# Optimization experiments

Measured on AMD Instinct MI355X. Metric: run time of the kernel, lower is better.

## Reference

```python
import jax, jax.numpy as jnp
import numpy as np

B, S, D, H, DH = 4, 2048, 1024, 16, 64
INIT_STD = 0.02
IGNORE = -100000.0


def setup_inputs() -> dict:
    key = jax.random.key(0)
    ks = jax.random.split(key, 5)
    x = jax.random.normal(ks[0], (B, S, D), dtype=jnp.float32)
    W_Q = INIT_STD * jax.random.normal(ks[1], (H, D, DH), dtype=jnp.float32)
    W_K = INIT_STD * jax.random.normal(ks[2], (H, D, DH), dtype=jnp.float32)
    W_V = INIT_STD * jax.random.normal(ks[3], (H, D, DH), dtype=jnp.float32)
    W_O = INIT_STD * jax.random.normal(ks[4], (H, DH, D), dtype=jnp.float32)
    b_Q = jnp.zeros((H, DH), dtype=jnp.float32)
    b_K = jnp.zeros((H, DH), dtype=jnp.float32)
    b_V = jnp.zeros((H, DH), dtype=jnp.float32)
    b_O = jnp.zeros((D,), dtype=jnp.float32)
    return {"x": x, "W_Q": W_Q, "b_Q": b_Q, "W_K": W_K, "b_K": b_K,
            "W_V": W_V, "b_V": b_V, "W_O": W_O, "b_O": b_O}


def reference(x, W_Q, b_Q, W_K, b_K, W_V, b_V, W_O, b_O):
    # x: (B, S, D); projections -> (B, S, H, DH)
    Q = jnp.einsum('bqd,hde->bqhe', x, W_Q) + b_Q
    K = jnp.einsum('bkd,hde->bkhe', x, W_K) + b_K
    V = jnp.einsum('bkd,hde->bkhe', x, W_V) + b_V
    d_head = Q.shape[-1]
    # scores: (B, H, Sq, Sk)
    scores = jnp.einsum('bqhe,bkhe->bhqk', Q, K) / np.sqrt(d_head).astype(np.float32)
    s = scores.shape[-1]
    causal = jnp.triu(jnp.ones((s, s), dtype=bool), k=1)
    scores = jnp.where(causal, jnp.float32(IGNORE), scores)
    A = jax.nn.softmax(scores, axis=-1)
    z = jnp.einsum('bhqk,bkhe->bqhe', A, V)
    # output projection: sum over heads + bias
    attn_out = jnp.einsum('bqhe,hed->bqd', z, W_O) + b_O
    return attn_out
```

## Files before the change

### kernel.cpp

```cpp
#include <hip/hip_runtime.h>


#define B_ 4
#define S_ 2048
#define D_ 1024
#define H_ 16
#define DH_ 64

typedef unsigned short ushort_t;
typedef __attribute__((ext_vector_type(4))) short short4v;
typedef __attribute__((ext_vector_type(8))) short short8v;
typedef __attribute__((ext_vector_type(4))) float floatx4;
typedef __attribute__((ext_vector_type(4))) unsigned short ushort4v;

static __device__ __forceinline__ ushort_t f2bf(float f) {
    union { float f; unsigned u; } v; v.f = f;
    unsigned r = v.u + 0x7fffu + ((v.u >> 16) & 1u);
    return (ushort_t)(r >> 16);
}

static __device__ __forceinline__ float fast_exp2(float x) {
#if __has_builtin(__builtin_amdgcn_exp2f)
    return __builtin_amdgcn_exp2f(x);
#else
    return exp2f(x);
#endif
}

static __device__ __forceinline__ unsigned pack_bf16_tr(float lo, float hi) {
    union { float f; unsigned u; } a, b;
    a.f = lo; b.f = hi;
    return __builtin_amdgcn_perm(b.u, a.u, 0x07060302u);
}

static __device__ __forceinline__ void g2lds16(const void* g, void* l) {
    __builtin_amdgcn_global_load_lds(
        (__attribute__((address_space(1))) void*)(unsigned long long)(size_t)g,
        (__attribute__((address_space(3))) void*)(unsigned int)(size_t)l,
        16, 0, 0);
}

__global__ void prep_kernel(const float* __restrict__ x,
                            const float* __restrict__ wq, const float* __restrict__ wk,
                            const float* __restrict__ wv, const float* __restrict__ wo,
                            ushort_t* __restrict__ xb, ushort_t* __restrict__ wt,
                            ushort_t* __restrict__ wot) {
    __shared__ float tile[32][33];
    int bid = blockIdx.x;
    int tid = threadIdx.x;
    if (bid < 8192) {
        int i = (bid * 256 + tid) * 4;
        float4 v = *(const float4*)&x[i];
        ushort4v o;
        o[0] = f2bf(v.x); o[1] = f2bf(v.y); o[2] = f2bf(v.z); o[3] = f2bf(v.w);
        *(ushort4v*)&xb[i] = o;
        return;
    }
    const float* src;
    ushort_t* d;
    int C, r0, c0;
    if (bid < 11264) {
        int t = bid - 8192;
        int z = t / 64, r = t % 64;
        src = (z < 16 ? wq : (z < 32 ? wk : wv)) + (size_t)(z & 15) * 65536;
        d = wt + (size_t)z * 65536;
        C = 64; r0 = (r >> 1) * 32; c0 = (r & 1) * 32;
    } else {
        int t = bid - 11264;
        int z = t / 64, r = t % 64;
        src = wo + (size_t)z * 65536;
        d = wot + (size_t)z * 64;
        C = 1024; r0 = (r & 1) * 32; c0 = (r >> 1) * 32;
    }
    int tx = tid & 31, ty = tid >> 5;
#pragma unroll
    for (int i = 0; i < 4; ++i)
        tile[ty + i * 8][tx] = src[(size_t)(r0 + ty + i * 8) * C + c0 + tx];
    __syncthreads();
#pragma unroll
    for (int i = 0; i < 4; ++i)
        d[(size_t)(c0 + ty + i * 8) * 1024 + r0 + tx] = f2bf(tile[tx][ty + i * 8]);
}


#define GQ_BAR() __builtin_amdgcn_s_barrier()
#define GQ_VM4 do { asm volatile("s_waitcnt vmcnt(4)"); __builtin_amdgcn_sched_barrier(0); } while (0)
#define GQ_VM2 do { asm volatile("s_waitcnt vmcnt(2)"); __builtin_amdgcn_sched_barrier(0); } while (0)
#define GQ_VM0 do { asm volatile("s_waitcnt vmcnt(0)"); __builtin_amdgcn_sched_barrier(0); } while (0)
#define GQ_WAITLG do { asm volatile("s_waitcnt lgkmcnt(0)"); __builtin_amdgcn_sched_barrier(0); } while (0)

#define GQ_READS_B(KB)                                                          \
    _Pragma("unroll") for (int nt = 0; nt < 4; ++nt)                            \
        bfr[KB][nt] = *(const short8v*)&cB[(wn * 64 + nt * 16) * 64 + ((KB) ? kb1 : kb0)];

#define GQ_READS_A(MH, KB)                                                      \
    _Pragma("unroll") for (int i = 0; i < 2; ++i)                               \
        af[i] = *(const short8v*)&cA[(wm * 64 + ((MH) * 2 + i) * 16) * 64 + ((KB) ? kb1 : kb0)];

#define GQ_MFMA(MH, KB)                                                         \
    GQ_WAITLG;                                                                  \
    __builtin_amdgcn_s_setprio(1);                                              \
    _Pragma("unroll") for (int i = 0; i < 2; ++i)                               \
        _Pragma("unroll") for (int nt = 0; nt < 4; ++nt)                        \
            acc[(MH) * 2 + i][nt] = __builtin_amdgcn_mfma_f32_16x16x32_bf16(    \
                af[i], bfr[KB][nt], acc[(MH) * 2 + i][nt], 0, 0, 0);            \
    __builtin_amdgcn_s_setprio(0);                                              \
    __builtin_amdgcn_sched_barrier(0);

#define GQ_KSTEP(CA, CB, S1, S2, S3, S4, WMID, WEND) do {                       \
    const ushort_t* cA = (CA); const ushort_t* cB = (CB);                       \
    short8v af[2]; short8v bfr[2][4];                                           \
    GQ_READS_B(0) GQ_READS_A(0, 0) S1; GQ_BAR();                                \
    GQ_MFMA(0, 0) GQ_BAR();                                                     \
    GQ_READS_B(1) GQ_READS_A(0, 1) S2; GQ_BAR();                                \
    GQ_MFMA(0, 1) WMID; GQ_BAR();                                               \
    GQ_READS_A(1, 0) S3; GQ_BAR();                                              \
    GQ_MFMA(1, 0) GQ_BAR();                                                     \
    GQ_READS_A(1, 1) S4; GQ_BAR();                                              \
    GQ_MFMA(1, 1) WEND; GQ_BAR();                                               \
} while (0)

#define GQ_RUN()                                                                \
    stA(sA[0], 0, uA); stA(sA[0], 0, uA + 8);                                   \
    stB(sB[0], 0, bR); stB(sB[0], 0, bR + 8);                                   \
    stB(sB[0], 0, bR + 16); stB(sB[0], 0, bR + 24);                             \
    stA(sA[0], 0, uA + 32); stA(sA[0], 0, uA + 40);                             \
    GQ_VM2;                                                                     \
    GQ_BAR();                                                                   \
    int p = 0;                                                                  \
    for (int t = 0; t < 15; ++t) {                                              \
        const int kk = (t + 1) * 64;                                            \
        ushort_t* nA = sA[p ^ 1];                                               \
        ushort_t* nB = sB[p ^ 1];                                               \
        GQ_KSTEP(sA[p], sB[p],                                                  \
                 { stA(nA, kk, uA); stA(nA, kk, uA + 8); },                     \
                 { stB(nB, kk, bR); stB(nB, kk, bR + 8); },                     \
                 { stB(nB, kk, bR + 16); stB(nB, kk, bR + 24); },               \
                 { stA(nA, kk, uA + 32); stA(nA, kk, uA + 40); },               \
                 GQ_VM4, GQ_VM2);                                               \
        p ^= 1;                                                                 \
    }                                                                           \
    GQ_KSTEP(sA[1], sB[1], (void)0, (void)0, (void)0, (void)0, GQ_VM0, (void)0);

__global__ __launch_bounds__(256, 2) void gemm_qkv(const ushort_t* __restrict__ A,
                                                   const ushort_t* __restrict__ Wt,
                                                   const float* __restrict__ bq,
                                                   const float* __restrict__ bk,
                                                   const float* __restrict__ bv,
                                                   ushort_t* __restrict__ Qw,
                                                   ushort_t* __restrict__ Kw,
                                                   ushort_t* __restrict__ Vw) {
    __shared__ ushort_t sA[2][128 * 64];
    __shared__ ushort_t sB[2][128 * 64];
    const int tid = threadIdx.x;
    const int lane = tid & 63, w = tid >> 6;
    const int lq = lane & 15, quad = lane >> 4;
    const int wm = w >> 1, wn = w & 1;
    const int m0 = blockIdx.x * 128, n0 = blockIdx.y * 128;

    const int kb0 = lq * 64 + ((quad ^ (lq & 7)) << 3);
    const int kb1 = lq * 64 + (((4 | quad) ^ (lq & 7)) << 3);

    const int uA = ((w >> 1) << 6) + ((w & 1) << 4);
    const int bR = w * 32;

    auto stA = [&](ushort_t* dst, int kk, int R0) __attribute__((always_inline)) {
        int rr = R0 + (lane >> 3);
        int cc = (lane & 7) ^ (rr & 7);
        g2lds16(&A[(size_t)(m0 + rr) * 1024 + kk + cc * 8], &dst[R0 * 64]);
    };
    auto stB = [&](ushort_t* dst, int kk, int R0) __attribute__((always_inline)) {
        int rr = R0 + (lane >> 3);
        int cc = (lane & 7) ^ (rr & 7);
        g2lds16(&Wt[(size_t)(n0 + rr) * 1024 + kk + cc * 8], &dst[R0 * 64]);
    };

    floatx4 acc[4][4] = {};

    GQ_RUN()

    const int mat = blockIdx.y >> 3;
    const float* bias = mat == 0 ? bq : (mat == 1 ? bk : bv);
    const int colbase = (blockIdx.y & 7) * 128 + wn * 64;
    float bias_v[4];
#pragma unroll
    for (int nt = 0; nt < 4; ++nt) bias_v[nt] = bias[colbase + nt * 16 + lq];

#pragma unroll
    for (int mt = 0; mt < 4; ++mt) {
#pragma unroll
        for (int nt = 0; nt < 4; ++nt) {
            int row0 = m0 + wm * 64 + mt * 16 + quad * 4;
            int col = colbase + nt * 16 + lq;
            int h = col >> 6, e = col & 63;
            if (mat == 2) {
                int b = row0 >> 11, s = row0 & 2047;
                ushort4v pk;
#pragma unroll
                for (int rg = 0; rg < 4; ++rg) pk[rg] = f2bf(acc[mt][nt][rg] + bias_v[nt]);
                *(ushort4v*)&Vw[((size_t)((b << 4) | h) * 64 + e) * 2048 + s] = pk;
            } else {
                ushort_t* Du = mat == 0 ? Qw : Kw;
#pragma unroll
                for (int rg = 0; rg < 4; ++rg) {
                    int row = row0 + rg;
                    int b = row >> 11, s = row & 2047;
                    float v = acc[mt][nt][rg] + bias_v[nt];
                    if (mat == 0) v *= 0.18033688011112042f;
                    Du[((size_t)((b << 4) | h) * 2048 + s) * 64 + e] = f2bf(v);
                }
            }
        }
    }
}

__global__ __launch_bounds__(256) void attn_kernel(const ushort_t* __restrict__ Q,
                                                   const ushort_t* __restrict__ Kg,
                                                   const ushort_t* __restrict__ Vt,
                                                   ushort_t* __restrict__ Z) {
    __shared__ ushort_t sK[2][128 * 64];
    __shared__ ushort_t sV[2][64 * 128];
    const int tid = threadIdx.x;
    const int lane = tid & 63, w = tid >> 6;
    const int lq = lane & 15, quad = lane >> 4;
    const int bh = blockIdx.x;
    const int b = bh >> 4, h = bh & 15;
    const ushort_t* Qp = Q + (size_t)bh * S_ * DH_;
    const ushort_t* Kp = Kg + (size_t)bh * S_ * DH_;
    const ushort_t* Vp = Vt + (size_t)bh * DH_ * S_;

    const int kbase0 = lq * 64 + ((quad ^ (lq & 7)) << 3);
    const int kbase1 = lq * 64 + (((4 | quad) ^ (lq & 7)) << 3);
    const int vbase2 = lq * 128 + quad * 4;
    const int vko = (lq & 7) << 4;

    const floatx4 fzero = {0.f, 0.f, 0.f, 0.f};

    auto stageK = [&](int kt, int bs) __attribute__((always_inline)) {
        ushort_t* dK = sK[bs];
#pragma unroll
        for (int p = 0; p < 4; ++p) {
            int rrk = w * 32 + p * 8 + (lane >> 3);
            int ck = (lane & 7) ^ (rrk & 7);
            g2lds16(&Kp[(size_t)(kt * 128 + rrk) * 64 + ck * 8], &dK[(w * 32 + p * 8) * 64]);
        }
    };
    auto stageV = [&](int kt, int bs) __attribute__((always_inline)) {
        ushort_t* dV = sV[bs];
#pragma unroll
        for (int p = 0; p < 4; ++p) {
            int R0 = w * 16 + p * 4;
            int e = R0 + (lane >> 4);
            int u = lane & 15;
            int usw = ((((u >> 1) ^ (e & 7)) << 1) | (u & 1));
            g2lds16(&Vp[(size_t)e * 2048 + kt * 128 + usw * 8], &dV[R0 * 128]);
        }
    };

    for (int pass = 0; pass < 2; ++pass) {
        const int qt = pass == 0 ? (int)blockIdx.y : 15 - (int)blockIdx.y;
        const int q0 = qt * 128;

        short8v qf[2][2];
#pragma unroll
        for (int qi = 0; qi < 2; ++qi)
#pragma unroll
            for (int ks = 0; ks < 2; ++ks)
                qf[qi][ks] = *(const short8v*)&Qp[(size_t)(q0 + w * 32 + qi * 16 + lq) * DH_ + ks * 32 + quad * 8];

        float l_i[2] = {0.f, 0.f};
        floatx4 o[2][4] = {};

        __syncthreads();
        stageK(0, 0);
        stageV(0, 0);

        for (int kt = 0; kt <= qt; ++kt) {
            const bool diag = (kt == qt);
            const ushort_t* cK = sK[kt & 1];
            const ushort_t* cV = sV[kt & 1];

            __syncthreads();
            if (kt < qt) {
                stageK(kt + 1, (kt + 1) & 1);
                stageV(kt + 1, (kt + 1) & 1);
            }

            floatx4 st[8][2];
#pragma unroll
            for (int si = 0; si < 8; ++si) {
                short8v a0 = *(const short8v*)&cK[kbase0 + si * 1024];
                short8v a1 = *(const short8v*)&cK[kbase1 + si * 1024];
#pragma unroll
                for (int qi = 0; qi < 2; ++qi) {
                    st[si][qi] = __builtin_amdgcn_mfma_f32_16x16x32_bf16(a0, qf[qi][0], fzero, 0, 0, 0);
                    st[si][qi] = __builtin_amdgcn_mfma_f32_16x16x32_bf16(a1, qf[qi][1], st[si][qi], 0, 0, 0);
                }
            }

            short4v pf[8][2];
#pragma unroll
            for (int qi = 0; qi < 2; ++qi) {
                const int qg = q0 + w * 32 + qi * 16 + lq;
                float lsum = 0.f;
#pragma unroll
                for (int si = 0; si < 8; ++si) {
                    float p[4];
#pragma unroll
                    for (int rg = 0; rg < 4; ++rg) {
                        float v = st[si][qi][rg];
                        if (diag) {
                            int sg = kt * 128 + si * 16 + quad * 4 + rg;
                            if (sg > qg) v = -1e30f;
                        }
                        p[rg] = fast_exp2(v);
                        lsum += p[rg];
                    }
                    union { unsigned u[2]; short4v v4; } pk;
                    pk.u[0] = pack_bf16_tr(p[0], p[1]);
                    pk.u[1] = pack_bf16_tr(p[2], p[3]);
                    pf[si][qi] = pk.v4;
                }
                l_i[qi] += lsum;
            }

#pragma unroll
            for (int ksp = 0; ksp < 8; ++ksp) {
                const ushort_t* pV = &cV[vbase2 + ((ksp << 4) ^ vko)];
#pragma unroll
                for (int et = 0; et < 4; ++et) {
                    short4v vf = *(const short4v*)&pV[et * 2048];
#pragma unroll
                    for (int qi = 0; qi < 2; ++qi)
                        o[qi][et] = __builtin_amdgcn_mfma_f32_16x16x16bf16_1k(pf[ksp][qi], vf, o[qi][et], 0, 0, 0);
                }
            }
        }

#pragma unroll
        for (int qi = 0; qi < 2; ++qi) {
            float lf = l_i[qi];
            lf += __shfl_xor(lf, 16);
            lf += __shfl_xor(lf, 32);
            float linv[4];
#pragma unroll
            for (int rg = 0; rg < 4; ++rg) linv[rg] = 1.0f / __shfl(lf, quad * 4 + rg);
#pragma unroll
            for (int et = 0; et < 4; ++et) {
#pragma unroll
                for (int rg = 0; rg < 4; ++rg) {
                    int qg = q0 + w * 32 + qi * 16 + quad * 4 + rg;
                    int e = et * 16 + lq;
                    Z[((size_t)(b * S_ + qg) * H_ + h) * DH_ + e] = f2bf(o[qi][et][rg] * linv[rg]);
                }
            }
        }
    }
}

__global__ __launch_bounds__(256, 2) void gemm_o(const ushort_t* __restrict__ A,
                                                 const ushort_t* __restrict__ Bt,
                                                 const float* __restrict__ bias,
                                                 float* __restrict__ Dst) {
    __shared__ ushort_t sA[2][128 * 64];
    __shared__ ushort_t sB[2][128 * 64];
    const int tid = threadIdx.x;
    const int lane = tid & 63, w = tid >> 6;
    const int lq = lane & 15, quad = lane >> 4;
    const int wm = w >> 1, wn = w & 1;
    const int m0 = blockIdx.x * 128, n0 = blockIdx.y * 128;

    const int kb0 = lq * 64 + ((quad ^ (lq & 7)) << 3);
    const int kb1 = lq * 64 + (((4 | quad) ^ (lq & 7)) << 3);
    const int uA = ((w >> 1) << 6) + ((w & 1) << 4);
    const int bR = w * 32;

    auto stA = [&](ushort_t* dst, int kk, int R0) __attribute__((always_inline)) {
        int rr = R0 + (lane >> 3);
        int cc = (lane & 7) ^ (rr & 7);
        g2lds16(&A[(size_t)(m0 + rr) * 1024 + kk + cc * 8], &dst[R0 * 64]);
    };
    auto stB = [&](ushort_t* dst, int kk, int R0) __attribute__((always_inline)) {
        int rr = R0 + (lane >> 3);
        int cc = (lane & 7) ^ (rr & 7);
        g2lds16(&Bt[(size_t)(n0 + rr) * 1024 + kk + cc * 8], &dst[R0 * 64]);
    };

    floatx4 acc[4][4] = {};

    GQ_RUN()

    const int colbase = n0 + wn * 64;
    float bias_v[4];
#pragma unroll
    for (int nt = 0; nt < 4; ++nt) bias_v[nt] = bias[colbase + nt * 16 + lq];

#pragma unroll
    for (int mt = 0; mt < 4; ++mt) {
#pragma unroll
        for (int nt = 0; nt < 4; ++nt) {
            int row0 = m0 + wm * 64 + mt * 16 + quad * 4;
            int col = colbase + nt * 16 + lq;
#pragma unroll
            for (int rg = 0; rg < 4; ++rg)
                Dst[(size_t)(row0 + rg) * 1024 + col] = acc[mt][nt][rg] + bias_v[nt];
        }
    }
}

extern "C" void kernel_launch(void* const* d_in, const int* in_sizes, int n_in,
                              void* d_out, int out_size, void* d_ws, size_t ws_size,
                              hipStream_t stream) {
    const float* x  = (const float*)d_in[0];
    const float* wq = (const float*)d_in[1];
    const float* bq = (const float*)d_in[2];
    const float* wk = (const float*)d_in[3];
    const float* bk = (const float*)d_in[4];
    const float* wv = (const float*)d_in[5];
    const float* bv = (const float*)d_in[6];
    const float* wo = (const float*)d_in[7];
    const float* bo = (const float*)d_in[8];

    char* ws = (char*)d_ws;
    size_t off = 0;
    ushort_t* xb  = (ushort_t*)(ws + off); off += (size_t)8192 * 1024 * 2;
    ushort_t* wt  = (ushort_t*)(ws + off); off += (size_t)3 * 1024 * 1024 * 2;
    ushort_t* wot = (ushort_t*)(ws + off); off += (size_t)1024 * 1024 * 2;
    ushort_t* Qw  = (ushort_t*)(ws + off); off += (size_t)8192 * 1024 * 2;
    ushort_t* Kw  = (ushort_t*)(ws + off); off += (size_t)8192 * 1024 * 2;
    ushort_t* Vw  = (ushort_t*)(ws + off); off += (size_t)8192 * 1024 * 2;
    ushort_t* Zw  = (ushort_t*)(ws + off); off += (size_t)8192 * 1024 * 2;

    prep_kernel<<<12288, 256, 0, stream>>>(x, wq, wk, wv, wo, xb, wt, wot);
    gemm_qkv<<<dim3(64, 24), 256, 0, stream>>>(xb, wt, bq, bk, bv, Qw, Kw, Vw);
    attn_kernel<<<dim3(64, 8), 256, 0, stream>>>(Qw, Kw, Vw, Zw);
    gemm_o<<<dim3(64, 8), 256, 0, stream>>>(Zw, wot, bo, (float*)d_out);
}
```

Baseline: 246.7 us.

## Fuse fp32-to-bf16 conversion of x into QKV GEMM A-tile loading

Removes the separate conversion pass over x in the prep kernel and its bf16 workspace buffer; the QKV GEMM now loads fp32 x through registers, converts to bf16 and writes swizzled LDS tiles. This eliminates a full read/write pass of the activations. In exchange each GEMM block reads twice as many bytes for A, repeated across all column blocks, and loses the direct global-to-LDS path for A, raising register use and changing the pipeline's wait structure.

```diff
diff --git a/kernel.cpp b/kernel.cpp
--- a/kernel.cpp
+++ b/kernel.cpp
@@ -1,4 +1,8 @@
 #include <hip/hip_runtime.h>
+#if __has_include(<hip/hip_bf16.h>)
+#include <hip/hip_bf16.h>
+#define HAVE_HIP_BF16 1
+#endif
 
 
 #define B_ 4
@@ -17,6 +21,22 @@
     union { float f; unsigned u; } v; v.f = f;
     unsigned r = v.u + 0x7fffu + ((v.u >> 16) & 1u);
     return (ushort_t)(r >> 16);
+}
+
+static __device__ __forceinline__ short8v cvt8(float4 a, float4 b) {
+#ifdef HAVE_HIP_BF16
+    union { short8v v; __hip_bfloat162 h[4]; } r;
+    r.h[0] = __float22bfloat162_rn(make_float2(a.x, a.y));
+    r.h[1] = __float22bfloat162_rn(make_float2(a.z, a.w));
+    r.h[2] = __float22bfloat162_rn(make_float2(b.x, b.y));
+    r.h[3] = __float22bfloat162_rn(make_float2(b.z, b.w));
+    return r.v;
+#else
+    union { short8v v; ushort_t s[8]; } r;
+    r.s[0] = f2bf(a.x); r.s[1] = f2bf(a.y); r.s[2] = f2bf(a.z); r.s[3] = f2bf(a.w);
+    r.s[4] = f2bf(b.x); r.s[5] = f2bf(b.y); r.s[6] = f2bf(b.z); r.s[7] = f2bf(b.w);
+    return r.v;
+#endif
 }
 
 static __device__ __forceinline__ float fast_exp2(float x) {
@@ -40,33 +60,22 @@
         16, 0, 0);
 }
 
-__global__ void prep_kernel(const float* __restrict__ x,
-                            const float* __restrict__ wq, const float* __restrict__ wk,
+__global__ void prep_kernel(const float* __restrict__ wq, const float* __restrict__ wk,
                             const float* __restrict__ wv, const float* __restrict__ wo,
-                            ushort_t* __restrict__ xb, ushort_t* __restrict__ wt,
-                            ushort_t* __restrict__ wot) {
+                            ushort_t* __restrict__ wt, ushort_t* __restrict__ wot) {
     __shared__ float tile[32][33];
     int bid = blockIdx.x;
     int tid = threadIdx.x;
-    if (bid < 8192) {
-        int i = (bid * 256 + tid) * 4;
-        float4 v = *(const float4*)&x[i];
-        ushort4v o;
-        o[0] = f2bf(v.x); o[1] = f2bf(v.y); o[2] = f2bf(v.z); o[3] = f2bf(v.w);
-        *(ushort4v*)&xb[i] = o;
-        return;
-    }
     const float* src;
     ushort_t* d;
     int C, r0, c0;
-    if (bid < 11264) {
-        int t = bid - 8192;
-        int z = t / 64, r = t % 64;
+    if (bid < 3072) {
+        int z = bid / 64, r = bid % 64;
         src = (z < 16 ? wq : (z < 32 ? wk : wv)) + (size_t)(z & 15) * 65536;
         d = wt + (size_t)z * 65536;
         C = 64; r0 = (r >> 1) * 32; c0 = (r & 1) * 32;
     } else {
-        int t = bid - 11264;
+        int t = bid - 3072;
         int z = t / 64, r = t % 64;
         src = wo + (size_t)z * 65536;
         d = wot + (size_t)z * 64;
@@ -142,7 +151,7 @@
     }                                                                           \
     GQ_KSTEP(sA[1], sB[1], (void)0, (void)0, (void)0, (void)0, GQ_VM0, (void)0);
 
-__global__ __launch_bounds__(256, 2) void gemm_qkv(const ushort_t* __restrict__ A,
+__global__ __launch_bounds__(256, 2) void gemm_qkv(const float* __restrict__ X,
                                                    const ushort_t* __restrict__ Wt,
                                                    const float* __restrict__ bq,
                                                    const float* __restrict__ bk,
@@ -164,10 +173,29 @@
     const int uA = ((w >> 1) << 6) + ((w & 1) << 4);
     const int bR = w * 32;
 
-    auto stA = [&](ushort_t* dst, int kk, int R0) __attribute__((always_inline)) {
-        int rr = R0 + (lane >> 3);
-        int cc = (lane & 7) ^ (rr & 7);
-        g2lds16(&A[(size_t)(m0 + rr) * 1024 + kk + cc * 8], &dst[R0 * 64]);
+    const int arow = uA + (lane & 15);
+    const int ac8 = (lane >> 4) * 2;
+    const int asw0 = ((ac8 ^ (arow & 7)) << 3);
+    const int asw1 = (((ac8 + 1) ^ (arow & 7)) << 3);
+
+    float4 ald[8];
+    auto issueA = [&](int kk) __attribute__((always_inline)) {
+        const float* base = &X[(size_t)(m0 + arow) * 1024 + kk + ac8 * 8];
+        ald[0] = *(const float4*)base;
+        ald[1] = *(const float4*)(base + 4);
+        ald[2] = *(const float4*)(base + 8);
+        ald[3] = *(const float4*)(base + 12);
+        const float* lbase = base + 32 * 1024;
+        ald[4] = *(const float4*)lbase;
+        ald[5] = *(const float4*)(lbase + 4);
+        ald[6] = *(const float4*)(lbase + 8);
+        ald[7] = *(const float4*)(lbase + 12);
+    };
+    auto writeA = [&](ushort_t* dst) __attribute__((always_inline)) {
+        *(short8v*)&dst[arow * 64 + asw0] = cvt8(ald[0], ald[1]);
+        *(short8v*)&dst[arow * 64 + asw1] = cvt8(ald[2], ald[3]);
+        *(short8v*)&dst[(arow + 32) * 64 + asw0] = cvt8(ald[4], ald[5]);
+        *(short8v*)&dst[(arow + 32) * 64 + asw1] = cvt8(ald[6], ald[7]);
     };
     auto stB = [&](ushort_t* dst, int kk, int R0) __attribute__((always_inline)) {
         int rr = R0 + (lane >> 3);
@@ -177,7 +205,29 @@
 
     floatx4 acc[4][4] = {};
 
-    GQ_RUN()
+    issueA(0);
+    stB(sB[0], 0, bR); stB(sB[0], 0, bR + 8);
+    stB(sB[0], 0, bR + 16); stB(sB[0], 0, bR + 24);
+    GQ_VM4;
+    writeA(sA[0]);
+    GQ_WAITLG;
+    GQ_VM0;
+    GQ_BAR();
+
+    int p = 0;
+    for (int t = 0; t < 15; ++t) {
+        const int kk = (t + 1) * 64;
+        ushort_t* nA = sA[p ^ 1];
+        ushort_t* nB = sB[p ^ 1];
+        GQ_KSTEP(sA[p], sB[p],
+                 { issueA(kk); },
+                 { stB(nB, kk, bR); stB(nB, kk, bR + 8); },
+                 { stB(nB, kk, bR + 16); stB(nB, kk, bR + 24); GQ_VM4; writeA(nA); },
+                 { },
+                 (void)0, GQ_VM0);
+        p ^= 1;
+    }
+    GQ_KSTEP(sA[1], sB[1], (void)0, (void)0, (void)0, (void)0, (void)0, (void)0);
 
     const int mat = blockIdx.y >> 3;
     const float* bias = mat == 0 ? bq : (mat == 1 ? bk : bv);
@@ -423,7 +473,6 @@
 
     char* ws = (char*)d_ws;
     size_t off = 0;
-    ushort_t* xb  = (ushort_t*)(ws + off); off += (size_t)8192 * 1024 * 2;
     ushort_t* wt  = (ushort_t*)(ws + off); off += (size_t)3 * 1024 * 1024 * 2;
     ushort_t* wot = (ushort_t*)(ws + off); off += (size_t)1024 * 1024 * 2;
     ushort_t* Qw  = (ushort_t*)(ws + off); off += (size_t)8192 * 1024 * 2;
@@ -431,8 +480,8 @@
     ushort_t* Vw  = (ushort_t*)(ws + off); off += (size_t)8192 * 1024 * 2;
     ushort_t* Zw  = (ushort_t*)(ws + off); off += (size_t)8192 * 1024 * 2;
 
-    prep_kernel<<<12288, 256, 0, stream>>>(x, wq, wk, wv, wo, xb, wt, wot);
-    gemm_qkv<<<dim3(64, 24), 256, 0, stream>>>(xb, wt, bq, bk, bv, Qw, Kw, Vw);
+    prep_kernel<<<4096, 256, 0, stream>>>(wq, wk, wv, wo, wt, wot);
+    gemm_qkv<<<dim3(64, 24), 256, 0, stream>>>(x, wt, bq, bk, bv, Qw, Kw, Vw);
     attn_kernel<<<dim3(64, 8), 256, 0, stream>>>(Qw, Kw, Vw, Zw);
     gemm_o<<<dim3(64, 8), 256, 0, stream>>>(Zw, wot, bo, (float*)d_out);
 }
```

After: 301.8 us. 1.22x slower.

## Use eight waves per block in QKV GEMM with smaller per-wave tiles

Applied to the files above, without the earlier changes.

The QKV projection GEMM goes from 256 to 512 threads per block, splitting the 128x128 tile over a 2x4 wave grid so each wave computes 64x32 instead of 64x64. The global-to-LDS loads are redistributed so each wave issues fewer copies per k-step, with waitcnt thresholds adjusted to match. This aims to raise the number of resident waves and hide latency better, at the cost of fewer MFMAs per LDS read and more barrier traffic per wave.

```diff
diff --git a/kernel.cpp b/kernel.cpp
--- a/kernel.cpp
+++ b/kernel.cpp
@@ -85,7 +85,9 @@
 
 #define GQ_BAR() __builtin_amdgcn_s_barrier()
 #define GQ_VM4 do { asm volatile("s_waitcnt vmcnt(4)"); __builtin_amdgcn_sched_barrier(0); } while (0)
+#define GQ_VM3 do { asm volatile("s_waitcnt vmcnt(3)"); __builtin_amdgcn_sched_barrier(0); } while (0)
 #define GQ_VM2 do { asm volatile("s_waitcnt vmcnt(2)"); __builtin_amdgcn_sched_barrier(0); } while (0)
+#define GQ_VM1 do { asm volatile("s_waitcnt vmcnt(1)"); __builtin_amdgcn_sched_barrier(0); } while (0)
 #define GQ_VM0 do { asm volatile("s_waitcnt vmcnt(0)"); __builtin_amdgcn_sched_barrier(0); } while (0)
 #define GQ_WAITLG do { asm volatile("s_waitcnt lgkmcnt(0)"); __builtin_amdgcn_sched_barrier(0); } while (0)
 
@@ -142,7 +144,38 @@
     }                                                                           \
     GQ_KSTEP(sA[1], sB[1], (void)0, (void)0, (void)0, (void)0, GQ_VM0, (void)0);
 
-__global__ __launch_bounds__(256, 2) void gemm_qkv(const ushort_t* __restrict__ A,
+#define GQ8_READS_B(KB)                                                         \
+    _Pragma("unroll") for (int nt = 0; nt < 2; ++nt)                            \
+        bfr[KB][nt] = *(const short8v*)&cB[(wn * 32 + nt * 16) * 64 + ((KB) ? kb1 : kb0)];
+
+#define GQ8_READS_A(MH, KB)                                                     \
+    _Pragma("unroll") for (int i = 0; i < 2; ++i)                               \
+        af[i] = *(const short8v*)&cA[(wm * 64 + ((MH) * 2 + i) * 16) * 64 + ((KB) ? kb1 : kb0)];
+
+#define GQ8_MFMA(MH, KB)                                                        \
+    GQ_WAITLG;                                                                  \
+    __builtin_amdgcn_s_setprio(1);                                              \
+    _Pragma("unroll") for (int i = 0; i < 2; ++i)                               \
+        _Pragma("unroll") for (int nt = 0; nt < 2; ++nt)                        \
+            acc[(MH) * 2 + i][nt] = __builtin_amdgcn_mfma_f32_16x16x32_bf16(    \
+                af[i], bfr[KB][nt], acc[(MH) * 2 + i][nt], 0, 0, 0);            \
+    __builtin_amdgcn_s_setprio(0);                                              \
+    __builtin_amdgcn_sched_barrier(0);
+
+#define GQ8_KSTEP(CA, CB, S1, S2, S3, WMID, WEND) do {                          \
+    const ushort_t* cA = (CA); const ushort_t* cB = (CB);                       \
+    short8v af[2]; short8v bfr[2][2];                                           \
+    GQ8_READS_B(0) GQ8_READS_A(0, 0) S1; GQ_BAR();                              \
+    GQ8_MFMA(0, 0) GQ_BAR();                                                    \
+    GQ8_READS_B(1) GQ8_READS_A(0, 1) S2; GQ_BAR();                              \
+    GQ8_MFMA(0, 1) WMID; GQ_BAR();                                              \
+    GQ8_READS_A(1, 0) S3; GQ_BAR();                                             \
+    GQ8_MFMA(1, 0) GQ_BAR();                                                    \
+    GQ8_READS_A(1, 1) GQ_BAR();                                                 \
+    GQ8_MFMA(1, 1) WEND; GQ_BAR();                                              \
+} while (0)
+
+__global__ __launch_bounds__(512, 2) void gemm_qkv(const ushort_t* __restrict__ A,
                                                    const ushort_t* __restrict__ Wt,
                                                    const float* __restrict__ bq,
                                                    const float* __restrict__ bk,
@@ -155,14 +188,14 @@
     const int tid = threadIdx.x;
     const int lane = tid & 63, w = tid >> 6;
     const int lq = lane & 15, quad = lane >> 4;
-    const int wm = w >> 1, wn = w & 1;
+    const int wm = w >> 2, wn = w & 3;
     const int m0 = blockIdx.x * 128, n0 = blockIdx.y * 128;
 
     const int kb0 = lq * 64 + ((quad ^ (lq & 7)) << 3);
     const int kb1 = lq * 64 + (((4 | quad) ^ (lq & 7)) << 3);
 
-    const int uA = ((w >> 1) << 6) + ((w & 1) << 4);
-    const int bR = w * 32;
+    const int uA = ((w >> 2) << 6) + ((w & 3) << 3);
+    const int bR = w * 16;
 
     auto stA = [&](ushort_t* dst, int kk, int R0) __attribute__((always_inline)) {
         int rr = R0 + (lane >> 3);
@@ -175,21 +208,39 @@
         g2lds16(&Wt[(size_t)(n0 + rr) * 1024 + kk + cc * 8], &dst[R0 * 64]);
     };
 
-    floatx4 acc[4][4] = {};
-
-    GQ_RUN()
+    floatx4 acc[4][2] = {};
+
+    stA(sA[0], 0, uA);
+    stB(sB[0], 0, bR); stB(sB[0], 0, bR + 8);
+    stA(sA[0], 0, uA + 32);
+    GQ_VM1;
+    GQ_BAR();
+
+    int p = 0;
+    for (int t = 0; t < 15; ++t) {
+        const int kk = (t + 1) * 64;
+        ushort_t* nA = sA[p ^ 1];
+        ushort_t* nB = sB[p ^ 1];
+        GQ8_KSTEP(sA[p], sB[p],
+                  { stA(nA, kk, uA); },
+                  { stB(nB, kk, bR); stB(nB, kk, bR + 8); },
+                  { stA(nA, kk, uA + 32); },
+                  GQ_VM3, GQ_VM1);
+        p ^= 1;
+    }
+    GQ8_KSTEP(sA[1], sB[1], (void)0, (void)0, (void)0, GQ_VM0, (void)0);
 
     const int mat = blockIdx.y >> 3;
     const float* bias = mat == 0 ? bq : (mat == 1 ? bk : bv);
-    const int colbase = (blockIdx.y & 7) * 128 + wn * 64;
-    float bias_v[4];
-#pragma unroll
-    for (int nt = 0; nt < 4; ++nt) bias_v[nt] = bias[colbase + nt * 16 + lq];
+    const int colbase = (blockIdx.y & 7) * 128 + wn * 32;
+    float bias_v[2];
+#pragma unroll
+    for (int nt = 0; nt < 2; ++nt) bias_v[nt] = bias[colbase + nt * 16 + lq];
 
 #pragma unroll
     for (int mt = 0; mt < 4; ++mt) {
 #pragma unroll
-        for (int nt = 0; nt < 4; ++nt) {
+        for (int nt = 0; nt < 2; ++nt) {
             int row0 = m0 + wm * 64 + mt * 16 + quad * 4;
             int col = colbase + nt * 16 + lq;
             int h = col >> 6, e = col & 63;
@@ -432,7 +483,7 @@
     ushort_t* Zw  = (ushort_t*)(ws + off); off += (size_t)8192 * 1024 * 2;
 
     prep_kernel<<<12288, 256, 0, stream>>>(x, wq, wk, wv, wo, xb, wt, wot);
-    gemm_qkv<<<dim3(64, 24), 256, 0, stream>>>(xb, wt, bq, bk, bv, Qw, Kw, Vw);
+    gemm_qkv<<<dim3(64, 24), 512, 0, stream>>>(xb, wt, bq, bk, bv, Qw, Kw, Vw);
     attn_kernel<<<dim3(64, 8), 256, 0, stream>>>(Qw, Kw, Vw, Zw);
     gemm_o<<<dim3(64, 8), 256, 0, stream>>>(Zw, wot, bo, (float*)d_out);
 }
```

New measurement: 240.2 us. 1.03x faster.
